# Kernel optimization log

Hardware: AMD Instinct MI355X
Metric: run time of the kernel (lower is better)

Reference implementation:

```python
import jax, jax.numpy as jnp
import numpy as np

L, D, H, DK, DFF = 6, 768, 12, 64, 3072
VOCAB, NUM_BUCKETS, MAX_DIST = 32128, 32, 128
B, S = 8, 512
NEG = -1e9


def t5_layer_norm(x, w, eps=1e-6):
    var = jnp.mean(jnp.square(x), axis=-1, keepdims=True)
    return w * x * jax.lax.rsqrt(var + eps)


def relative_position_bucket(rel, num_buckets=NUM_BUCKETS, max_distance=MAX_DIST):
    # bidirectional T5 bucketing
    nb = num_buckets // 2
    ret = (rel > 0).astype(jnp.int32) * nb
    n = jnp.abs(rel)
    max_exact = nb // 2
    is_small = n < max_exact
    logf = jnp.log(jnp.maximum(n, 1).astype(jnp.float32) / max_exact)
    val_large = max_exact + (logf / np.log(max_distance / max_exact) * (nb - max_exact)).astype(jnp.int32)
    val_large = jnp.minimum(val_large, nb - 1)
    return ret + jnp.where(is_small, n, val_large)


def setup_inputs() -> dict:
    key = jax.random.key(0)
    ks = jax.random.split(key, 9)
    w = 0.02  # weight scale for numeric stability over 6 blocks
    return {
        "input_ids": jax.random.randint(ks[0], (B, S), 0, VOCAB),
        "attention_mask": jnp.ones((B, S), jnp.float32),
        "embed_w": jax.random.normal(ks[1], (VOCAB, D), jnp.float32),
        "ln1_w": jnp.ones((L, D), jnp.float32),
        "q_w": jax.random.normal(ks[2], (L, H * DK, D), jnp.float32) * w,
        "k_w": jax.random.normal(ks[3], (L, H * DK, D), jnp.float32) * w,
        "v_w": jax.random.normal(ks[4], (L, H * DK, D), jnp.float32) * w,
        "rel_bias_w": jax.random.normal(ks[5], (NUM_BUCKETS, H), jnp.float32),
        "o_w": jax.random.normal(ks[6], (L, D, H * DK), jnp.float32) * w,
        "ln2_w": jnp.ones((L, D), jnp.float32),
        "wi_w": jax.random.normal(ks[7], (L, DFF, D), jnp.float32) * w,
        "wo_w": jax.random.normal(ks[8], (L, D, DFF), jnp.float32) * w,
        "final_ln_w": jnp.ones((D,), jnp.float32),
    }


def reference(input_ids, attention_mask, embed_w, ln1_w, q_w, k_w, v_w,
              rel_bias_w, o_w, ln2_w, wi_w, wo_w, final_ln_w):
    b, s = input_ids.shape
    h = embed_w[input_ids]  # [B,S,D]

    # position bias computed once (block 0 owns the table; shared by all blocks)
    pos = jnp.arange(s)
    rel = pos[None, :] - pos[:, None]  # memory - query, [S,S]
    bucket = relative_position_bucket(rel)
    pos_bias = rel_bias_w[bucket]  # [S,S,H]
    pos_bias = jnp.transpose(pos_bias, (2, 0, 1))[None]  # [1,H,S,S]
    ext_mask = (1.0 - attention_mask)[:, None, None, :] * NEG  # [B,1,1,S]
    bias = pos_bias + ext_mask  # [B,H,S,S]

    for l in range(L):
        # --- self-attention (T5: no 1/sqrt(d) scaling) ---
        x = t5_layer_norm(h, ln1_w[l])
        q = jnp.einsum('bsd,id->bsi', x, q_w[l]).reshape(b, s, H, DK).transpose(0, 2, 1, 3)
        k = jnp.einsum('bsd,id->bsi', x, k_w[l]).reshape(b, s, H, DK).transpose(0, 2, 1, 3)
        v = jnp.einsum('bsd,id->bsi', x, v_w[l]).reshape(b, s, H, DK).transpose(0, 2, 1, 3)
        scores = jnp.einsum('bhqd,bhkd->bhqk', q, k) + bias
        attn = jax.nn.softmax(scores, axis=-1)
        ctx = jnp.einsum('bhqk,bhkd->bhqd', attn, v)
        ctx = ctx.transpose(0, 2, 1, 3).reshape(b, s, H * DK)
        h = h + jnp.einsum('bsi,di->bsd', ctx, o_w[l])
        # --- ReLU FFN ---
        x = t5_layer_norm(h, ln2_w[l])
        ff = jax.nn.relu(jnp.einsum('bsd,fd->bsf', x, wi_w[l]))
        h = h + jnp.einsum('bsf,df->bsd', ff, wo_w[l])

    return t5_layer_norm(h, final_ln_w)
```

## Files before the change

### kernel.cpp

```cpp
#include <hip/hip_runtime.h>
#include <hip/hip_bf16.h>
#include <math.h>

#define L_ 6
#define D_ 768
#define H_ 12
#define DK_ 64
#define DFF_ 3072
#define NB_ 32
#define MAXDIST_ 128
#define B_ 8
#define S_ 512
#define NEG_ (-1e9f)
#define BS_ (B_*S_)
#define BSD_ ((size_t)BS_*D_)
#define WLAYER_ 7077888

typedef __bf16 bf16x8 __attribute__((ext_vector_type(8)));
typedef float f32x4 __attribute__((ext_vector_type(4)));

__device__ __forceinline__ unsigned short f2bf(float f) {
    unsigned u = __float_as_uint(f);
    u += 0x7fff + ((u >> 16) & 1);
    return (unsigned short)(u >> 16);
}
__device__ __forceinline__ float bf2f(unsigned short s) {
    return __uint_as_float(((unsigned)s) << 16);
}

#define GLDS(g, l) __builtin_amdgcn_global_load_lds( \
    (const __attribute__((address_space(1))) void*)(const void*)(g), \
    (__attribute__((address_space(3))) void*)(void*)(l), 16, 0, 0)

__global__ __launch_bounds__(192) void k_embed(const int* __restrict__ ids,
                                               const float* __restrict__ ew,
                                               float* __restrict__ h) {
    int row = blockIdx.x;
    int id = ids[row];
    const float4* src = (const float4*)(ew + (size_t)id * D_);
    float4* dst = (float4*)(h + (size_t)row * D_);
    dst[threadIdx.x] = src[threadIdx.x];
}

template<int OUTBF>
__global__ __launch_bounds__(256) void k_rmsnorm(const float* __restrict__ in,
                                                 const float* __restrict__ w,
                                                 void* __restrict__ outp) {
    int row = blockIdx.x;
    int tid = threadIdx.x;
    const float* x = in + (size_t)row * D_;
    float ss = 0.f;
    for (int i = tid; i < D_; i += 256) { float v = x[i]; ss += v * v; }
    #pragma unroll
    for (int off = 32; off; off >>= 1) ss += __shfl_down(ss, off, 64);
    __shared__ float sbuf[4];
    if ((tid & 63) == 0) sbuf[tid >> 6] = ss;
    __syncthreads();
    float tot = sbuf[0] + sbuf[1] + sbuf[2] + sbuf[3];
    float scale = rsqrtf(tot / (float)D_ + 1e-6f);
    if (OUTBF) {
        unsigned short* o = (unsigned short*)outp + (size_t)row * D_;
        for (int i = tid; i < D_; i += 256) o[i] = f2bf(w[i] * x[i] * scale);
    } else {
        float* o = (float*)outp + (size_t)row * D_;
        for (int i = tid; i < D_; i += 256) o[i] = w[i] * x[i] * scale;
    }
}

__global__ __launch_bounds__(256) void k_posbias(const float* __restrict__ rbw,
                                                 unsigned short* __restrict__ biasg) {
    int idx = blockIdx.x * 256 + threadIdx.x;
    if (idx >= S_ * S_) return;
    int q = idx / S_, key = idx - q * S_;
    int rel = key - q;
    const int nb = NB_ / 2;
    int ret = rel > 0 ? nb : 0;
    int n = rel < 0 ? -rel : rel;
    const int max_exact = nb / 2;
    int val;
    if (n < max_exact) {
        val = n;
    } else {
        float lf = logf((float)n / (float)max_exact) /
                   logf((float)MAXDIST_ / (float)max_exact) * (float)(nb - max_exact);
        val = max_exact + (int)lf;
        if (val > nb - 1) val = nb - 1;
    }
    int bucket = ret + val;
    #pragma unroll
    for (int hh = 0; hh < H_; ++hh)
        biasg[((size_t)hh * S_ + q) * S_ + key] = f2bf(rbw[bucket * H_ + hh]);
}

#define W1V8 73728
#define W2V8 294912
#define WLV8 884736
__global__ __launch_bounds__(256) void k_wconv_all(const float* __restrict__ qw,
                                                   const float* __restrict__ kw,
                                                   const float* __restrict__ vw,
                                                   const float* __restrict__ ow,
                                                   const float* __restrict__ wiw,
                                                   const float* __restrict__ wow,
                                                   unsigned short* __restrict__ wb) {
    int gid = blockIdx.x * 256 + threadIdx.x;
    int l = gid / WLV8;
    int i = gid - l * WLV8;
    const float* src;
    if (i < W1V8)                src = qw  + (size_t)l * 589824;
    else if ((i -= W1V8) < W1V8) src = kw  + (size_t)l * 589824;
    else if ((i -= W1V8) < W1V8) src = vw  + (size_t)l * 589824;
    else if ((i -= W1V8) < W1V8) src = ow  + (size_t)l * 589824;
    else if ((i -= W1V8) < W2V8) src = wiw + (size_t)l * 2359296;
    else { i -= W2V8;            src = wow + (size_t)l * 2359296; }
    const float4* s4 = (const float4*)src + (size_t)i * 2;
    float4 a = s4[0], b = s4[1];
    ushort4 lo, hi;
    lo.x = f2bf(a.x); lo.y = f2bf(a.y); lo.z = f2bf(a.z); lo.w = f2bf(a.w);
    hi.x = f2bf(b.x); hi.y = f2bf(b.y); hi.z = f2bf(b.z); hi.w = f2bf(b.w);
    ushort4* d = (ushort4*)(wb + (size_t)gid * 8);
    d[0] = lo; d[1] = hi;
}

template<int BM, int BN>
__device__ __forceinline__ void stage_tile_t(const unsigned short* __restrict__ Abase,
                                             const unsigned short* __restrict__ Bbase,
                                             int k0, int K, int buf,
                                             unsigned short* lsA, unsigned short* lsB,
                                             int w, int lane) {
    constexpr int CA = BM / 32, CB = BN / 32;
    #pragma unroll
    for (int c = 0; c < CA; ++c) {
        int off = c * 4096 + w * 1024 + lane * 16;
        int row = off >> 7;
        int sc = (off & 127) ^ ((row & 7) << 4);
        GLDS(Abase + (size_t)row * K + k0 + (sc >> 1), (char*)lsA + buf * (BM * 128) + off);
    }
    #pragma unroll
    for (int c = 0; c < CB; ++c) {
        int off = c * 4096 + w * 1024 + lane * 16;
        int row = off >> 7;
        int sc = (off & 127) ^ ((row & 7) << 4);
        GLDS(Bbase + (size_t)row * K + k0 + (sc >> 1), (char*)lsB + buf * (BN * 128) + off);
    }
}

template<int BM, int BN>
__device__ __forceinline__ void gemm_compute_t(const char* cA, const char* cB,
                                               f32x4 acc[BM / 32][BN / 32],
                                               int l15, int l4, int wr, int wc) {
    constexpr int MI = BM / 32, NJ = BN / 32;
    #pragma unroll
    for (int kk = 0; kk < 2; ++kk) {
        bf16x8 af[MI], bfr[NJ];
        int kByte = kk * 64 + l4 * 16;
        #pragma unroll
        for (int i = 0; i < MI; ++i) {
            int r = wr + i * 16 + l15;
            af[i] = *(const bf16x8*)(cA + r * 128 + (kByte ^ ((r & 7) << 4)));
        }
        #pragma unroll
        for (int j = 0; j < NJ; ++j) {
            int r = wc + j * 16 + l15;
            bfr[j] = *(const bf16x8*)(cB + r * 128 + (kByte ^ ((r & 7) << 4)));
        }
        #pragma unroll
        for (int i = 0; i < MI; ++i)
            #pragma unroll
            for (int j = 0; j < NJ; ++j)
                acc[i][j] = __builtin_amdgcn_mfma_f32_16x16x32_bf16(af[i], bfr[j], acc[i][j], 0, 0, 0);
    }
}

template<int BM, int BN>
__device__ __forceinline__ void gemm_core_t(const unsigned short* __restrict__ A,
                                            const unsigned short* __restrict__ Bw,
                                            int K, int bm, int bn,
                                            unsigned short* lsA, unsigned short* lsB,
                                            f32x4 acc[BM / 32][BN / 32]) {
    int t = threadIdx.x, lane = t & 63, w = t >> 6;
    int l15 = lane & 15, l4 = lane >> 4;
    int wr = (w >> 1) * (BM / 2), wc = (w & 1) * (BN / 2);
    const unsigned short* Abase = A + (size_t)(bm * BM) * K;
    const unsigned short* Bbase = Bw + (size_t)(bn * BN) * K;
    int nt = K >> 6;
    constexpr int NL = BM / 32 + BN / 32;

    stage_tile_t<BM, BN>(Abase, Bbase, 0, K, 0, lsA, lsB, w, lane);
    for (int tq = 0; tq < nt - 1; ++tq) {
        int cur = tq & 1;
        stage_tile_t<BM, BN>(Abase, Bbase, (tq + 1) << 6, K, cur ^ 1, lsA, lsB, w, lane);
        if constexpr (NL == 8)      asm volatile("s_waitcnt vmcnt(8)" ::: "memory");
        else if constexpr (NL == 6) asm volatile("s_waitcnt vmcnt(6)" ::: "memory");
        else                        asm volatile("s_waitcnt vmcnt(4)" ::: "memory");
        __builtin_amdgcn_s_barrier();
        gemm_compute_t<BM, BN>((const char*)lsA + cur * (BM * 128),
                               (const char*)lsB + cur * (BN * 128), acc, l15, l4, wr, wc);
        asm volatile("s_waitcnt lgkmcnt(0)" ::: "memory");
        __builtin_amdgcn_s_barrier();
    }
    int cur = (nt - 1) & 1;
    asm volatile("s_waitcnt vmcnt(0)" ::: "memory");
    __builtin_amdgcn_s_barrier();
    gemm_compute_t<BM, BN>((const char*)lsA + cur * (BM * 128),
                           (const char*)lsB + cur * (BN * 128), acc, l15, l4, wr, wc);
}

template<int BM, int BN, int RES, int RELU, int OUTBF>
__global__ __launch_bounds__(256) void k_gemm_t(const unsigned short* __restrict__ A,
                                                const unsigned short* __restrict__ Bw,
                                                const float* __restrict__ res,
                                                void* __restrict__ C, int N, int K) {
    __shared__ __align__(16) unsigned short lsA[2 * BM * 64];
    __shared__ __align__(16) unsigned short lsB[2 * BN * 64];
    f32x4 acc[BM / 32][BN / 32] = {};
    int bm = blockIdx.x, bn = blockIdx.y;
    gemm_core_t<BM, BN>(A, Bw, K, bm, bn, lsA, lsB, acc);
    int t = threadIdx.x, lane = t & 63, w = t >> 6;
    int l15 = lane & 15, l4 = lane >> 4;
    int wr = (w >> 1) * (BM / 2), wc = (w & 1) * (BN / 2);
    #pragma unroll
    for (int i = 0; i < BM / 32; ++i) {
        #pragma unroll
        for (int r = 0; r < 4; ++r) {
            int row = bm * BM + wr + i * 16 + l4 * 4 + r;
            #pragma unroll
            for (int j = 0; j < BN / 32; ++j) {
                int col = bn * BN + wc + j * 16 + l15;
                float v = acc[i][j][r];
                if (RES)  v += res[(size_t)row * N + col];
                if (RELU) v = fmaxf(v, 0.f);
                if (OUTBF) ((unsigned short*)C)[(size_t)row * N + col] = f2bf(v);
                else       ((float*)C)[(size_t)row * N + col] = v;
            }
        }
    }
}

__global__ __launch_bounds__(256) void k_gemm_qkv_bf(const unsigned short* __restrict__ X,
                                                     const unsigned short* __restrict__ wq,
                                                     const unsigned short* __restrict__ wk,
                                                     const unsigned short* __restrict__ wv,
                                                     unsigned short* __restrict__ qo,
                                                     unsigned short* __restrict__ ko,
                                                     unsigned short* __restrict__ vt) {
    __shared__ __align__(16) unsigned short lsA[2 * 64 * 64];
    __shared__ __align__(16) unsigned short lsB[2 * 128 * 64];
    f32x4 acc[2][4] = {};
    int z = blockIdx.z;
    const unsigned short* Bm = z == 0 ? wq : (z == 1 ? wk : wv);
    int bm = blockIdx.x, bn = blockIdx.y;
    gemm_core_t<64, 128>(X, Bm, D_, bm, bn, lsA, lsB, acc);
    int t = threadIdx.x, lane = t & 63, w = t >> 6;
    int l15 = lane & 15, l4 = lane >> 4;
    int wr = (w >> 1) * 32, wc = (w & 1) * 64;
    if (z < 2) {
        unsigned short* C = z == 0 ? qo : ko;
        #pragma unroll
        for (int i = 0; i < 2; ++i)
            #pragma unroll
            for (int r = 0; r < 4; ++r) {
                int row = bm * 64 + wr + i * 16 + l4 * 4 + r;
                #pragma unroll
                for (int j = 0; j < 4; ++j) {
                    int col = bn * 128 + wc + j * 16 + l15;
                    C[(size_t)row * D_ + col] = f2bf(acc[i][j][r]);
                }
            }
    } else {
        #pragma unroll
        for (int i = 0; i < 2; ++i) {
            int row0 = bm * 64 + wr + i * 16 + l4 * 4;
            int b = row0 >> 9, s0 = row0 & 511;
            #pragma unroll
            for (int j = 0; j < 4; ++j) {
                int col = bn * 128 + wc + j * 16 + l15;
                int hh = col >> 6, dv = col & 63;
                ushort4 o4;
                o4.x = f2bf(acc[i][j][0]); o4.y = f2bf(acc[i][j][1]);
                o4.z = f2bf(acc[i][j][2]); o4.w = f2bf(acc[i][j][3]);
                *(ushort4*)(vt + (((size_t)b * H_ + hh) * 64 + dv) * S_ + s0) = o4;
            }
        }
    }
}

__global__ __launch_bounds__(256) void k_attn_flash(const unsigned short* __restrict__ qb,
                                                    const unsigned short* __restrict__ kb,
                                                    const unsigned short* __restrict__ vtb,
                                                    const unsigned short* __restrict__ biasg,
                                                    const float* __restrict__ mask,
                                                    unsigned short* __restrict__ ctx) {
    __shared__ __align__(16) unsigned short Kt[64 * 64];
    __shared__ __align__(16) unsigned short Vt[64 * 64];
    __shared__ __align__(16) unsigned short Bt[64 * 64];
    __shared__ __align__(16) unsigned short Pt[4][16 * 64];

    int t = threadIdx.x, lane = t & 63, w = t >> 6;
    int l15 = lane & 15, l4 = lane >> 4;
    int bh = blockIdx.y;
    int b = bh / H_, hh = bh - b * H_;
    int qblk = blockIdx.x;
    int qloc = w * 16 + l15;
    int qg = qblk * 64 + qloc;

    bf16x8 qf[2];
    {
        const unsigned short* qp = qb + ((size_t)(b * S_ + qg)) * D_ + hh * DK_;
        qf[0] = *(const bf16x8*)(qp + l4 * 8);
        qf[1] = *(const bf16x8*)(qp + 32 + l4 * 8);
    }
    float mrun = -1e30f, lsum = 0.f;
    f32x4 cacc[4] = {};

    for (int kt = 0; kt < S_ / 64; ++kt) {
        int kbase = kt * 64;
        __syncthreads();
        #pragma unroll
        for (int c = 0; c < 2; ++c) {
            int off = (w * 2 + c) * 1024 + lane * 16;
            int row = off >> 7;
            int colb = (off & 127) ^ ((row & 7) << 4);
            GLDS(kb + ((size_t)(b * S_ + kbase + row)) * D_ + hh * DK_ + (colb >> 1),
                 (char*)Kt + off);
            GLDS(vtb + ((size_t)bh * 64 + row) * S_ + kbase + (colb >> 1),
                 (char*)Vt + off);
            GLDS(biasg + ((size_t)hh * S_ + qblk * 64 + row) * S_ + kbase + (colb >> 1),
                 (char*)Bt + off);
        }
        __syncthreads();

        f32x4 sc[4] = {};
        #pragma unroll
        for (int kk = 0; kk < 2; ++kk) {
            int kByte = kk * 64 + l4 * 16;
            #pragma unroll
            for (int j = 0; j < 4; ++j) {
                int r = j * 16 + l15;
                bf16x8 kf = *(const bf16x8*)((const char*)Kt + r * 128 + (kByte ^ ((r & 7) << 4)));
                sc[j] = __builtin_amdgcn_mfma_f32_16x16x32_bf16(kf, qf[kk], sc[j], 0, 0, 0);
            }
        }
        float sv[4][4];
        float tmax = -1e30f;
        #pragma unroll
        for (int j = 0; j < 4; ++j) {
            int bro = qloc * 128 + ((j * 32 + l4 * 8) ^ ((qloc & 7) << 4));
            ushort4 b4 = *(const ushort4*)((const char*)Bt + bro);
            float4 m4 = *(const float4*)(mask + (size_t)b * S_ + kbase + j * 16 + l4 * 4);
            sv[j][0] = sc[j][0] + bf2f(b4.x) + (1.f - m4.x) * NEG_;
            sv[j][1] = sc[j][1] + bf2f(b4.y) + (1.f - m4.y) * NEG_;
            sv[j][2] = sc[j][2] + bf2f(b4.z) + (1.f - m4.z) * NEG_;
            sv[j][3] = sc[j][3] + bf2f(b4.w) + (1.f - m4.w) * NEG_;
            tmax = fmaxf(tmax, fmaxf(fmaxf(sv[j][0], sv[j][1]), fmaxf(sv[j][2], sv[j][3])));
        }
        tmax = fmaxf(tmax, __shfl_xor(tmax, 16, 64));
        tmax = fmaxf(tmax, __shfl_xor(tmax, 32, 64));
        float mnew = fmaxf(mrun, tmax);
        float scal = __expf(mrun - mnew);
        #pragma unroll
        for (int i = 0; i < 4; ++i) {
            cacc[i][0] *= scal; cacc[i][1] *= scal;
            cacc[i][2] *= scal; cacc[i][3] *= scal;
        }
        float psum = 0.f;
        unsigned pp[8];
        #pragma unroll
        for (int j = 0; j < 4; ++j) {
            float p0 = __expf(sv[j][0] - mnew), p1 = __expf(sv[j][1] - mnew);
            float p2 = __expf(sv[j][2] - mnew), p3 = __expf(sv[j][3] - mnew);
            psum += (p0 + p1) + (p2 + p3);
            pp[j * 2]     = (unsigned)f2bf(p0) | ((unsigned)f2bf(p1) << 16);
            pp[j * 2 + 1] = (unsigned)f2bf(p2) | ((unsigned)f2bf(p3) << 16);
        }
        lsum = lsum * scal + psum;
        mrun = mnew;
        unsigned short* P = Pt[w];
        #pragma unroll
        for (int j = 0; j < 4; ++j) {
            int base = l15 * 128 + ((j * 32 + l4 * 8) ^ ((l15 & 7) << 4));
            *(unsigned*)((char*)P + base) = pp[j * 2];
            *(unsigned*)((char*)P + base + 4) = pp[j * 2 + 1];
        }
        #pragma unroll
        for (int kk = 0; kk < 2; ++kk) {
            int kByte = kk * 64 + l4 * 16;
            bf16x8 pf = *(const bf16x8*)((const char*)P + l15 * 128 + (kByte ^ ((l15 & 7) << 4)));
            #pragma unroll
            for (int i = 0; i < 4; ++i) {
                int rr = i * 16 + l15;
                bf16x8 vf = *(const bf16x8*)((const char*)Vt + rr * 128 + (kByte ^ ((rr & 7) << 4)));
                cacc[i] = __builtin_amdgcn_mfma_f32_16x16x32_bf16(vf, pf, cacc[i], 0, 0, 0);
            }
        }
    }
    lsum += __shfl_xor(lsum, 16, 64);
    lsum += __shfl_xor(lsum, 32, 64);
    float inv = 1.f / lsum;
    unsigned short* cp = ctx + ((size_t)(b * S_ + qg)) * D_ + hh * DK_;
    #pragma unroll
    for (int i = 0; i < 4; ++i) {
        ushort4 o4;
        o4.x = f2bf(cacc[i][0] * inv); o4.y = f2bf(cacc[i][1] * inv);
        o4.z = f2bf(cacc[i][2] * inv); o4.w = f2bf(cacc[i][3] * inv);
        *(ushort4*)(cp + i * 16 + l4 * 4) = o4;
    }
}

extern "C" void kernel_launch(void* const* d_in, const int* in_sizes, int n_in,
                              void* d_out, int out_size, void* d_ws, size_t ws_size,
                              hipStream_t stream) {
    const int*   ids  = (const int*)d_in[0];
    const float* mask = (const float*)d_in[1];
    const float* ew   = (const float*)d_in[2];
    const float* ln1  = (const float*)d_in[3];
    const float* qw   = (const float*)d_in[4];
    const float* kw   = (const float*)d_in[5];
    const float* vw   = (const float*)d_in[6];
    const float* rbw  = (const float*)d_in[7];
    const float* ow   = (const float*)d_in[8];
    const float* ln2  = (const float*)d_in[9];
    const float* wiw  = (const float*)d_in[10];
    const float* wow  = (const float*)d_in[11];
    const float* flnw = (const float*)d_in[12];
    float* out = (float*)d_out;

    char* p = (char*)d_ws;
    float* h = (float*)p;                        p += BSD_ * 4;
    unsigned short* biasg = (unsigned short*)p;  p += (size_t)H_ * S_ * S_ * 2;
    unsigned short* wball = (unsigned short*)p;  p += (size_t)L_ * WLAYER_ * 2;
    unsigned short* xbf   = (unsigned short*)p;  p += BSD_ * 2;
    unsigned short* ctxb  = xbf;
    unsigned short* qbB   = (unsigned short*)p;  p += BSD_ * 2;
    unsigned short* kbB   = (unsigned short*)p;  p += BSD_ * 2;
    unsigned short* vtb   = (unsigned short*)p;  p += BSD_ * 2;
                    p += BSD_ * 2;
    unsigned short* ff    = qbB;

    k_embed<<<BS_, 192, 0, stream>>>(ids, ew, h);
    k_posbias<<<(S_ * S_ + 255) / 256, 256, 0, stream>>>(rbw, biasg);
    k_wconv_all<<<(L_ * WLV8) / 256, 256, 0, stream>>>(qw, kw, vw, ow, wiw, wow, wball);

    for (int l = 0; l < L_; ++l) {
        const unsigned short* wl  = wball + (size_t)l * WLAYER_;
        const unsigned short* wq  = wl;
        const unsigned short* wk  = wl + 589824;
        const unsigned short* wv  = wl + 1179648;
        const unsigned short* wo  = wl + 1769472;
        const unsigned short* wwi = wl + 2359296;
        const unsigned short* wwo = wl + 4718592;

        k_rmsnorm<1><<<BS_, 256, 0, stream>>>(h, ln1 + (size_t)l * D_, xbf);
        k_gemm_qkv_bf<<<dim3(BS_ / 64, D_ / 128, 3), 256, 0, stream>>>(
            xbf, wq, wk, wv, qbB, kbB, vtb);
        k_attn_flash<<<dim3(S_ / 64, B_ * H_), 256, 0, stream>>>(
            qbB, kbB, vtb, biasg, mask, ctxb);
        k_gemm_t<64, 64, 1, 0, 0><<<dim3(BS_ / 64, D_ / 64), 256, 0, stream>>>(
            ctxb, wo, h, h, D_, D_);
        k_rmsnorm<1><<<BS_, 256, 0, stream>>>(h, ln2 + (size_t)l * D_, xbf);
        k_gemm_t<64, 128, 0, 1, 1><<<dim3(BS_ / 64, DFF_ / 128), 256, 0, stream>>>(
            xbf, wwi, nullptr, ff, DFF_, D_);
        k_gemm_t<64, 64, 1, 0, 0><<<dim3(BS_ / 64, D_ / 64), 256, 0, stream>>>(
            ff, wwo, h, h, D_, DFF_);
    }
    k_rmsnorm<0><<<BS_, 256, 0, stream>>>(h, flnw, out);
}
```

Baseline: 879.0 us.

## Double-buffer K/V tiles in flash attention and read bias directly from global

The attention kernel now double-buffers the K and V tiles in LDS, issuing the next tile's async global-to-LDS loads before computing on the current one and waiting with explicit vmcnt counts. The positional bias is read straight from global into registers instead of being staged through LDS. MFMA sections are also wrapped in s_setprio raises. The weight-conversion kernel is changed to process 4 floats per thread instead of 8. The aim is to hide global load latency behind compute in attention, in exchange for more LDS per block and reliance on hand-tuned waitcnt values.

```diff
diff --git a/kernel.cpp b/kernel.cpp
--- a/kernel.cpp
+++ b/kernel.cpp
@@ -92,9 +92,9 @@
         biasg[((size_t)hh * S_ + q) * S_ + key] = f2bf(rbw[bucket * H_ + hh]);
 }
 
-#define W1V8 73728
-#define W2V8 294912
-#define WLV8 884736
+#define W1V4 147456
+#define W2V4 589824
+#define WLV4 1769472
 __global__ __launch_bounds__(256) void k_wconv_all(const float* __restrict__ qw,
                                                    const float* __restrict__ kw,
                                                    const float* __restrict__ vw,
@@ -103,22 +103,19 @@
                                                    const float* __restrict__ wow,
                                                    unsigned short* __restrict__ wb) {
     int gid = blockIdx.x * 256 + threadIdx.x;
-    int l = gid / WLV8;
-    int i = gid - l * WLV8;
+    int l = gid / WLV4;
+    int i = gid - l * WLV4;
     const float* src;
-    if (i < W1V8)                src = qw  + (size_t)l * 589824;
-    else if ((i -= W1V8) < W1V8) src = kw  + (size_t)l * 589824;
-    else if ((i -= W1V8) < W1V8) src = vw  + (size_t)l * 589824;
-    else if ((i -= W1V8) < W1V8) src = ow  + (size_t)l * 589824;
-    else if ((i -= W1V8) < W2V8) src = wiw + (size_t)l * 2359296;
-    else { i -= W2V8;            src = wow + (size_t)l * 2359296; }
-    const float4* s4 = (const float4*)src + (size_t)i * 2;
-    float4 a = s4[0], b = s4[1];
-    ushort4 lo, hi;
-    lo.x = f2bf(a.x); lo.y = f2bf(a.y); lo.z = f2bf(a.z); lo.w = f2bf(a.w);
-    hi.x = f2bf(b.x); hi.y = f2bf(b.y); hi.z = f2bf(b.z); hi.w = f2bf(b.w);
-    ushort4* d = (ushort4*)(wb + (size_t)gid * 8);
-    d[0] = lo; d[1] = hi;
+    if (i < W1V4)                src = qw  + (size_t)l * 589824;
+    else if ((i -= W1V4) < W1V4) src = kw  + (size_t)l * 589824;
+    else if ((i -= W1V4) < W1V4) src = vw  + (size_t)l * 589824;
+    else if ((i -= W1V4) < W1V4) src = ow  + (size_t)l * 589824;
+    else if ((i -= W1V4) < W2V4) src = wiw + (size_t)l * 2359296;
+    else { i -= W2V4;            src = wow + (size_t)l * 2359296; }
+    float4 a = ((const float4*)src)[i];
+    ushort4 o4;
+    o4.x = f2bf(a.x); o4.y = f2bf(a.y); o4.z = f2bf(a.z); o4.w = f2bf(a.w);
+    ((ushort4*)wb)[gid] = o4;
 }
 
 template<int BM, int BN>
@@ -290,9 +287,8 @@
                                                     const unsigned short* __restrict__ biasg,
                                                     const float* __restrict__ mask,
                                                     unsigned short* __restrict__ ctx) {
-    __shared__ __align__(16) unsigned short Kt[64 * 64];
-    __shared__ __align__(16) unsigned short Vt[64 * 64];
-    __shared__ __align__(16) unsigned short Bt[64 * 64];
+    __shared__ __align__(16) unsigned short Kt[2][64 * 64];
+    __shared__ __align__(16) unsigned short Vt[2][64 * 64];
     __shared__ __align__(16) unsigned short Pt[4][16 * 64];
 
     int t = threadIdx.x, lane = t & 63, w = t >> 6;
@@ -312,45 +308,63 @@
     float mrun = -1e30f, lsum = 0.f;
     f32x4 cacc[4] = {};
 
-    for (int kt = 0; kt < S_ / 64; ++kt) {
+    auto stage_kv = [&](int kt, int buf) {
         int kbase = kt * 64;
-        __syncthreads();
         #pragma unroll
         for (int c = 0; c < 2; ++c) {
             int off = (w * 2 + c) * 1024 + lane * 16;
             int row = off >> 7;
             int colb = (off & 127) ^ ((row & 7) << 4);
             GLDS(kb + ((size_t)(b * S_ + kbase + row)) * D_ + hh * DK_ + (colb >> 1),
-                 (char*)Kt + off);
+                 (char*)Kt[buf] + off);
             GLDS(vtb + ((size_t)bh * 64 + row) * S_ + kbase + (colb >> 1),
-                 (char*)Vt + off);
-            GLDS(biasg + ((size_t)hh * S_ + qblk * 64 + row) * S_ + kbase + (colb >> 1),
-                 (char*)Bt + off);
-        }
-        __syncthreads();
+                 (char*)Vt[buf] + off);
+        }
+    };
+
+    stage_kv(0, 0);
+    const unsigned short* bprow = biasg + ((size_t)hh * S_ + qblk * 64 + qloc) * S_;
+
+    for (int kt = 0; kt < S_ / 64; ++kt) {
+        int cur = kt & 1;
+        int kbase = kt * 64;
+        ushort4 b4[4];
+        float4 m4[4];
+        #pragma unroll
+        for (int j = 0; j < 4; ++j) {
+            b4[j] = *(const ushort4*)(bprow + kbase + j * 16 + l4 * 4);
+            m4[j] = *(const float4*)(mask + (size_t)b * S_ + kbase + j * 16 + l4 * 4);
+        }
+        if (kt < S_ / 64 - 1) {
+            stage_kv(kt + 1, cur ^ 1);
+            asm volatile("s_waitcnt vmcnt(4)" ::: "memory");
+        } else {
+            asm volatile("s_waitcnt vmcnt(0)" ::: "memory");
+        }
+        __builtin_amdgcn_s_barrier();
 
         f32x4 sc[4] = {};
+        __builtin_amdgcn_s_setprio(1);
         #pragma unroll
         for (int kk = 0; kk < 2; ++kk) {
             int kByte = kk * 64 + l4 * 16;
             #pragma unroll
             for (int j = 0; j < 4; ++j) {
                 int r = j * 16 + l15;
-                bf16x8 kf = *(const bf16x8*)((const char*)Kt + r * 128 + (kByte ^ ((r & 7) << 4)));
+                bf16x8 kf = *(const bf16x8*)((const char*)Kt[cur] + r * 128 + (kByte ^ ((r & 7) << 4)));
                 sc[j] = __builtin_amdgcn_mfma_f32_16x16x32_bf16(kf, qf[kk], sc[j], 0, 0, 0);
             }
         }
+        __builtin_amdgcn_s_setprio(0);
+
         float sv[4][4];
         float tmax = -1e30f;
         #pragma unroll
         for (int j = 0; j < 4; ++j) {
-            int bro = qloc * 128 + ((j * 32 + l4 * 8) ^ ((qloc & 7) << 4));
-            ushort4 b4 = *(const ushort4*)((const char*)Bt + bro);
-            float4 m4 = *(const float4*)(mask + (size_t)b * S_ + kbase + j * 16 + l4 * 4);
-            sv[j][0] = sc[j][0] + bf2f(b4.x) + (1.f - m4.x) * NEG_;
-            sv[j][1] = sc[j][1] + bf2f(b4.y) + (1.f - m4.y) * NEG_;
-            sv[j][2] = sc[j][2] + bf2f(b4.z) + (1.f - m4.z) * NEG_;
-            sv[j][3] = sc[j][3] + bf2f(b4.w) + (1.f - m4.w) * NEG_;
+            sv[j][0] = sc[j][0] + bf2f(b4[j].x) + (1.f - m4[j].x) * NEG_;
+            sv[j][1] = sc[j][1] + bf2f(b4[j].y) + (1.f - m4[j].y) * NEG_;
+            sv[j][2] = sc[j][2] + bf2f(b4[j].z) + (1.f - m4[j].z) * NEG_;
+            sv[j][3] = sc[j][3] + bf2f(b4[j].w) + (1.f - m4[j].w) * NEG_;
             tmax = fmaxf(tmax, fmaxf(fmaxf(sv[j][0], sv[j][1]), fmaxf(sv[j][2], sv[j][3])));
         }
         tmax = fmaxf(tmax, __shfl_xor(tmax, 16, 64));
@@ -381,6 +395,7 @@
             *(unsigned*)((char*)P + base) = pp[j * 2];
             *(unsigned*)((char*)P + base + 4) = pp[j * 2 + 1];
         }
+        __builtin_amdgcn_s_setprio(1);
         #pragma unroll
         for (int kk = 0; kk < 2; ++kk) {
             int kByte = kk * 64 + l4 * 16;
@@ -388,10 +403,13 @@
             #pragma unroll
             for (int i = 0; i < 4; ++i) {
                 int rr = i * 16 + l15;
-                bf16x8 vf = *(const bf16x8*)((const char*)Vt + rr * 128 + (kByte ^ ((rr & 7) << 4)));
+                bf16x8 vf = *(const bf16x8*)((const char*)Vt[cur] + rr * 128 + (kByte ^ ((rr & 7) << 4)));
                 cacc[i] = __builtin_amdgcn_mfma_f32_16x16x32_bf16(vf, pf, cacc[i], 0, 0, 0);
             }
         }
+        __builtin_amdgcn_s_setprio(0);
+        asm volatile("s_waitcnt lgkmcnt(0)" ::: "memory");
+        __builtin_amdgcn_s_barrier();
     }
     lsum += __shfl_xor(lsum, 16, 64);
     lsum += __shfl_xor(lsum, 32, 64);
@@ -438,7 +456,7 @@
 
     k_embed<<<BS_, 192, 0, stream>>>(ids, ew, h);
     k_posbias<<<(S_ * S_ + 255) / 256, 256, 0, stream>>>(rbw, biasg);
-    k_wconv_all<<<(L_ * WLV8) / 256, 256, 0, stream>>>(qw, kw, vw, ow, wiw, wow, wball);
+    k_wconv_all<<<(L_ * WLV4) / 256, 256, 0, stream>>>(qw, kw, vw, ow, wiw, wow, wball);
 
     for (int l = 0; l < L_; ++l) {
         const unsigned short* wl  = wball + (size_t)l * WLAYER_;
```

Result: no change. 892.7 us (+1.6%).
